# Kernel optimization log

Measured on AMD Instinct MI355X. Metric: run time of the kernel, lower is better.

Reference implementation:

```python
import jax, jax.numpy as jnp
import numpy as np

B_, N, C = 1024, 64, 512
H = 16          # num_heads
NW = 64         # number of windows (B_ % NW == 0)


def setup_inputs() -> dict:
    key = jax.random.key(0)
    ks = jax.random.split(key, 7)
    return {
        "x": jax.random.normal(ks[0], (B_, N, C), jnp.float32),
        "mask": jax.random.normal(ks[1], (NW, N, N), jnp.float32),
        "qkv_w": jax.random.normal(ks[2], (C, 3 * C), jnp.float32) * 0.02,
        "qkv_b": jax.random.normal(ks[3], (3 * C,), jnp.float32) * 0.02,
        "proj_w": jax.random.normal(ks[4], (C, C), jnp.float32) * 0.02,
        "proj_b": jax.random.normal(ks[5], (C,), jnp.float32) * 0.02,
        "bias_table": jax.random.normal(ks[6], (2 * N - 1, H), jnp.float32) * 0.02,
    }


def reference(x, mask, qkv_w, qkv_b, proj_w, proj_b, bias_table):
    b_, n, c = x.shape
    h = bias_table.shape[1]
    ws = (bias_table.shape[0] + 1) // 2  # window_size, == n here
    d = c // h
    scale = d ** -0.5

    qkv = x @ qkv_w + qkv_b                                   # [B_, N, 3C]
    qkv = qkv.reshape(b_, n, 3, h, d).transpose(2, 0, 3, 1, 4)  # [3, B_, H, N, d]
    q, k, v = qkv[0] * scale, qkv[1], qkv[2]

    attn = jnp.einsum('bhnd,bhmd->bhnm', q, k)                # [B_, H, N, N]

    coords = jnp.arange(ws)
    rel_idx = coords[:, None] - coords[None, :] + ws - 1       # [ws, ws]
    bias = bias_table[rel_idx].transpose(2, 0, 1)              # [H, ws, ws]
    attn = attn + bias[None]

    nw = mask.shape[0]
    attn = attn.reshape(b_ // nw, nw, h, n, n) + mask[None, :, None]
    attn = attn.reshape(-1, h, n, n)
    attn = jax.nn.softmax(attn, axis=-1)

    out = jnp.einsum('bhnm,bhmd->bhnd', attn, v)               # [B_, H, N, d]
    # Faithful to the TF code: v keeps a leading singleton dim after tf.split,
    # so attn@v is [1, B_, H, N, d]; perm [0,2,1,3,4] swaps B_ and H before
    # the final reshape to (B_, N, C).
    out = out[None].transpose(0, 2, 1, 3, 4).reshape(b_, n, c)
    return out @ proj_w + proj_b
```

## Files before the change

kernel.cpp:

```cpp
#include <hip/hip_runtime.h>
#include <hip/hip_bf16.h>
#include <stdint.h>

typedef __attribute__((ext_vector_type(4))) float f32x4;
typedef __attribute__((ext_vector_type(8))) short s16x8;

__device__ __forceinline__ short f2bf(float f) {
  union { float f; uint32_t u; } v; v.f = f;
  uint32_t r = v.u + 0x7FFFu + ((v.u >> 16) & 1u);
  return (short)(r >> 16);
}

__device__ __forceinline__ void async16(const void* g, void* l) {
  __builtin_amdgcn_global_load_lds(
      (const __attribute__((address_space(1))) void*)g,
      (__attribute__((address_space(3))) void*)l, 16, 0, 0);
}

__global__ __launch_bounds__(256) void k_cast_bf16(const float* __restrict__ in,
                                                   short* __restrict__ out, int n8) {
  int i = blockIdx.x * 256 + threadIdx.x;
  if (i >= n8) return;
  const float4* p = (const float4*)in + (size_t)i * 2;
  float4 a = p[0], b = p[1];
  s16x8 o;
  o[0] = f2bf(a.x); o[1] = f2bf(a.y); o[2] = f2bf(a.z); o[3] = f2bf(a.w);
  o[4] = f2bf(b.x); o[5] = f2bf(b.y); o[6] = f2bf(b.z); o[7] = f2bf(b.w);
  ((s16x8*)out)[i] = o;
}

__global__ __launch_bounds__(256) void k_transpose_cast(const float* __restrict__ in,
                                                        short* __restrict__ out,
                                                        int K, int N) {
  __shared__ float tile[64][65];
  const int bx = blockIdx.x;
  const int by = blockIdx.y;
  const int tx = threadIdx.x & 63, ty = threadIdx.x >> 6;
#pragma unroll
  for (int r = ty; r < 64; r += 4)
    tile[r][tx] = in[(size_t)(by * 64 + r) * N + bx * 64 + tx];
  __syncthreads();
#pragma unroll
  for (int r = ty; r < 64; r += 4)
    out[(size_t)(bx * 64 + r) * K + by * 64 + tx] = f2bf(tile[tx][r]);
}

#define TILE_SH 16384

template <bool F32OUT, int NBN>
__global__ __launch_bounds__(512, 2) void k_gemm256p(const short* __restrict__ A,
                                                     const short* __restrict__ Bw,
                                                     const float* __restrict__ bias,
                                                     void* __restrict__ C,
                                                     int N, int K, int nrounds) {
  __shared__ short lds[2 * 2 * TILE_SH];
  const int t = threadIdx.x;
  const int w = t >> 6, l = t & 63;
  const int wm = w >> 2, wn = w & 3;
  const int swz = (((int)blockIdx.x & 7) << 5) + ((int)blockIdx.x >> 3);

  const int NT = 8;
  const int NS = nrounds * NT;

  auto stage = [&](const short* __restrict__ G, int row0, int kt, short* dst) {
#pragma unroll
    for (int L = 0; L < 2; ++L) {
      int cw = L * 512 + (t & ~63);
      int c = cw + l;
      int r = c >> 3, s = c & 7;
      async16(G + (size_t)(row0 + r) * K + kt + ((s ^ (r & 7)) << 3), dst + cw * 8);
    }
  };
  auto issueA = [&](int step, int bmv, int hf) {
    int kt = step & 7;
    stage(A, bmv * 256 + hf * 128, kt * 64, lds + (kt & 1) * 32768 + hf * 8192);
  };
  auto issueB = [&](int step, int bnv, int hf) {
    int kt = step & 7;
    stage(Bw, bnv * 256 + hf * 128, kt * 64, lds + (kt & 1) * 32768 + TILE_SH + hf * 8192);
  };

  const int g = l >> 4, v = l & 7;
  int ofsA[2], ofsB[2];
#pragma unroll
  for (int ks = 0; ks < 2; ++ks) {
    ofsA[ks] = (wm * 128 + (l & 15)) * 64 + (((ks * 4 + g) ^ v) << 3);
    ofsB[ks] = (wn * 64 + (l & 15)) * 64 + (((ks * 4 + g) ^ v) << 3);
  }

  f32x4 acc[8][4] = {};
  s16x8 bfr[4][2];

  {
    const int bm0 = swz / NBN, bn0 = swz % NBN;
    issueB(0, bn0, 0); issueB(0, bn0, 1);
    issueA(0, bm0, 0); issueA(0, bm0, 1);
    issueB(1, bn0, 0); issueB(1, bn0, 1);
  }
  asm volatile("s_waitcnt vmcnt(4)" ::: "memory");
  __builtin_amdgcn_s_barrier();

#define PHASE(AI0, STAGE_STMT, TAIL_STMT)                                                                      \
  {                                                                                                            \
    s16x8 a00 = *(const s16x8*)(Ab + ofsA[0] + (AI0) * 1024);                                                  \
    s16x8 a01 = *(const s16x8*)(Ab + ofsA[1] + (AI0) * 1024);                                                  \
    s16x8 a10 = *(const s16x8*)(Ab + ofsA[0] + ((AI0) + 1) * 1024);                                            \
    s16x8 a11 = *(const s16x8*)(Ab + ofsA[1] + ((AI0) + 1) * 1024);                                            \
    STAGE_STMT;                                                                                                \
    __builtin_amdgcn_s_barrier();                                                                              \
    asm volatile("s_waitcnt lgkmcnt(0)" ::: "memory");                                                         \
    __builtin_amdgcn_s_setprio(1);                                                                             \
    _Pragma("unroll")                                                                                          \
    for (int nj = 0; nj < 4; ++nj) {                                                                           \
      acc[(AI0)][nj] = __builtin_amdgcn_mfma_f32_16x16x32_bf16(a00, bfr[nj][0], acc[(AI0)][nj], 0, 0, 0);      \
      acc[(AI0)][nj] = __builtin_amdgcn_mfma_f32_16x16x32_bf16(a01, bfr[nj][1], acc[(AI0)][nj], 0, 0, 0);      \
      acc[(AI0) + 1][nj] = __builtin_amdgcn_mfma_f32_16x16x32_bf16(a10, bfr[nj][0], acc[(AI0) + 1][nj], 0, 0, 0); \
      acc[(AI0) + 1][nj] = __builtin_amdgcn_mfma_f32_16x16x32_bf16(a11, bfr[nj][1], acc[(AI0) + 1][nj], 0, 0, 0); \
    }                                                                                                          \
    __builtin_amdgcn_s_setprio(0);                                                                             \
    TAIL_STMT;                                                                                                 \
    __builtin_amdgcn_s_barrier();                                                                              \
  }

  for (int j = 0; j < nrounds; ++j) {
    const int tauc = swz + (j << 8);
    const int bmc = tauc / NBN, bnc = tauc % NBN;
    for (int T = 0; T < NT; ++T) {
      const int s = (j << 3) + T;
      const int s1 = s + 1, s2 = s + 2;
      const int tau1 = swz + (((s1) >> 3) << 8);
      const int tau2 = swz + (((s2) >> 3) << 8);
      const int bm1 = tau1 / NBN;
      const int bn2 = tau2 % NBN;
      const short* Ab = lds + (T & 1) * 32768;
      const short* Bb = Ab + TILE_SH;
#pragma unroll
      for (int nj = 0; nj < 4; ++nj)
#pragma unroll
        for (int ks = 0; ks < 2; ++ks)
          bfr[nj][ks] = *(const s16x8*)(Bb + ofsB[ks] + nj * 1024);

      PHASE(0, if (s1 < NS) issueA(s1, bm1, 0), );
      PHASE(2, if (s1 < NS) issueA(s1, bm1, 1), );
      PHASE(4, if (s2 < NS) issueB(s2, bn2, 0), );
      PHASE(6, if (s2 < NS) issueB(s2, bn2, 1),
            if (s2 < NS) { asm volatile("s_waitcnt vmcnt(4)" ::: "memory"); }
            else if (s1 < NS) { asm volatile("s_waitcnt vmcnt(0)" ::: "memory"); });
    }

#pragma unroll
    for (int ai = 0; ai < 8; ++ai)
#pragma unroll
      for (int nj = 0; nj < 4; ++nj) {
        int col = bnc * 256 + wn * 64 + nj * 16 + (l & 15);
        float bv = bias[col];
#pragma unroll
        for (int r = 0; r < 4; ++r) {
          int row = bmc * 256 + wm * 128 + ai * 16 + (l >> 4) * 4 + r;
          float vv = acc[ai][nj][r] + bv;
          if (F32OUT)
            ((float*)C)[(size_t)row * N + col] = vv;
          else
            ((short*)C)[(size_t)row * N + col] = f2bf(vv);
        }
      }
#pragma unroll
    for (int ai = 0; ai < 8; ++ai)
#pragma unroll
      for (int nj = 0; nj < 4; ++nj)
        acc[ai][nj] = (f32x4){0.f, 0.f, 0.f, 0.f};
  }
#undef PHASE
}

__global__ __launch_bounds__(256) void k_attn(const short* __restrict__ qkv,
                                              const float* __restrict__ mask,
                                              const float* __restrict__ bias_table,
                                              short* __restrict__ Y) {
  __shared__ float mask_lds[64 * 64];
  __shared__ float bias_lds[4][128];
  __shared__ short p_lds[4][64][72];

  const int t = threadIdx.x, wv = t >> 6, ln = t & 63;
  const int b = blockIdx.x;
  const int h = blockIdx.y * 4 + wv;

  const float4* mk = (const float4*)(mask + (size_t)(b & 63) * 4096);
#pragma unroll
  for (int u = 0; u < 4; ++u)
    ((float4*)mask_lds)[t + 256 * u] = mk[t + 256 * u];
  for (int u = ln; u < 127; u += 64) bias_lds[wv][u] = bias_table[u * 16 + h];
  __syncthreads();

  const short* qb = qkv + (size_t)b * 64 * 1536 + h * 32;

  s16x8 qf[4], kf[4];
#pragma unroll
  for (int i = 0; i < 4; ++i) {
    qf[i] = *(const s16x8*)(qb + (size_t)(16 * i + (ln & 15)) * 1536 + (ln >> 4) * 8);
    kf[i] = *(const s16x8*)(qb + (size_t)(16 * i + (ln & 15)) * 1536 + 512 + (ln >> 4) * 8);
  }
  f32x4 s[4][4] = {};
#pragma unroll
  for (int i = 0; i < 4; ++i)
#pragma unroll
    for (int j = 0; j < 4; ++j)
      s[i][j] = __builtin_amdgcn_mfma_f32_16x16x32_bf16(qf[i], kf[j], s[i][j], 0, 0, 0);

  const float scale = 0.17677669529663687f;
#pragma unroll
  for (int i = 0; i < 4; ++i)
#pragma unroll
    for (int r = 0; r < 4; ++r) {
      int nn = 16 * i + (ln >> 4) * 4 + r;
      float vals[4];
      float vmax = -1e30f;
#pragma unroll
      for (int j = 0; j < 4; ++j) {
        int mm = 16 * j + (ln & 15);
        float x = s[i][j][r] * scale + bias_lds[wv][nn - mm + 63] + mask_lds[nn * 64 + mm];
        vals[j] = x;
        vmax = fmaxf(vmax, x);
      }
#pragma unroll
      for (int d = 1; d < 16; d <<= 1) vmax = fmaxf(vmax, __shfl_xor(vmax, d, 64));
      float sum = 0.f;
#pragma unroll
      for (int j = 0; j < 4; ++j) {
        float p = __expf(vals[j] - vmax);
        vals[j] = p;
        sum += p;
      }
#pragma unroll
      for (int d = 1; d < 16; d <<= 1) sum += __shfl_xor(sum, d, 64);
      float rsv = 1.0f / sum;
#pragma unroll
      for (int j = 0; j < 4; ++j)
        p_lds[wv][nn][16 * j + (ln & 15)] = f2bf(vals[j] * rsv);
    }

  const short* vg = qb + 1024;
  f32x4 o[4][2] = {};
#pragma unroll
  for (int kk = 0; kk < 2; ++kk) {
    s16x8 pa[4];
#pragma unroll
    for (int i2 = 0; i2 < 4; ++i2)
      pa[i2] = *(const s16x8*)&p_lds[wv][16 * i2 + (ln & 15)][kk * 32 + (ln >> 4) * 8];
#pragma unroll
    for (int j2 = 0; j2 < 2; ++j2) {
      s16x8 vf;
#pragma unroll
      for (int jj = 0; jj < 8; ++jj)
        vf[jj] = vg[(size_t)(kk * 32 + (ln >> 4) * 8 + jj) * 1536 + 16 * j2 + (ln & 15)];
#pragma unroll
      for (int i2 = 0; i2 < 4; ++i2)
        o[i2][j2] = __builtin_amdgcn_mfma_f32_16x16x32_bf16(pa[i2], vf, o[i2][j2], 0, 0, 0);
    }
  }

#pragma unroll
  for (int i2 = 0; i2 < 4; ++i2)
#pragma unroll
    for (int j2 = 0; j2 < 2; ++j2)
#pragma unroll
      for (int r = 0; r < 4; ++r) {
        int n = 16 * i2 + (ln >> 4) * 4 + r;
        int d = 16 * j2 + (ln & 15);
        int rr = h * 64 + (b >> 4);
        int ss = (b & 15) * 4 + (n >> 4);
        int cc = (n & 15) * 32 + d;
        Y[((size_t)rr * 64 + ss) * 512 + cc] = f2bf(o[i2][j2][r]);
      }
}

extern "C" void kernel_launch(void* const* d_in, const int* in_sizes, int n_in,
                              void* d_out, int out_size, void* d_ws, size_t ws_size,
                              hipStream_t stream) {
  const float* x      = (const float*)d_in[0];
  const float* mask   = (const float*)d_in[1];
  const float* qkv_w  = (const float*)d_in[2];
  const float* qkv_b  = (const float*)d_in[3];
  const float* proj_w = (const float*)d_in[4];
  const float* proj_b = (const float*)d_in[5];
  const float* btab   = (const float*)d_in[6];
  float* out = (float*)d_out;

  char* w = (char*)d_ws;
  short* qkv_ws = (short*)w;
  short* xbf    = (short*)(w + (size_t)65536 * 1536 * 2);
  short* Y      = xbf;
  short* wT     = (short*)(w + (size_t)65536 * 1536 * 2 + (size_t)65536 * 512 * 2);
  short* projT  = wT + 1536 * 512;

  k_cast_bf16<<<16384, 256, 0, stream>>>(x, xbf, 33554432 / 8);
  k_transpose_cast<<<dim3(24, 8), 256, 0, stream>>>(qkv_w, wT, 512, 1536);
  k_transpose_cast<<<dim3(8, 8), 256, 0, stream>>>(proj_w, projT, 512, 512);
  k_gemm256p<false, 6><<<256, 512, 0, stream>>>(xbf, wT, qkv_b, qkv_ws, 1536, 512, 6);
  k_attn<<<dim3(1024, 4), 256, 0, stream>>>(qkv_ws, mask, btab, Y);
  k_gemm256p<true, 2><<<256, 512, 0, stream>>>(Y, projT, proj_b, out, 512, 512, 2);
}
```

Before: 306.7 us.

## Restructure GEMM main loop into K-split half-tile double-buffered register pipeline

```diff
diff --git a/kernel.cpp b/kernel.cpp
--- a/kernel.cpp
+++ b/kernel.cpp
@@ -45,107 +45,100 @@
     out[(size_t)(bx * 64 + r) * K + by * 64 + tx] = f2bf(tile[tx][r]);
 }
 
-#define TILE_SH 16384
+#define RGN 16384
 
 template <bool F32OUT, int NBN>
-__global__ __launch_bounds__(512, 2) void k_gemm256p(const short* __restrict__ A,
-                                                     const short* __restrict__ Bw,
-                                                     const float* __restrict__ bias,
-                                                     void* __restrict__ C,
-                                                     int N, int K, int nrounds) {
-  __shared__ short lds[2 * 2 * TILE_SH];
+__global__ __launch_bounds__(512, 1) void k_gemmks(const short* __restrict__ A,
+                                                   const short* __restrict__ Bw,
+                                                   const float* __restrict__ bias,
+                                                   void* __restrict__ C,
+                                                   int N, int K, int nrounds) {
+  __shared__ short lds[4 * RGN];
   const int t = threadIdx.x;
   const int w = t >> 6, l = t & 63;
   const int wm = w >> 2, wn = w & 3;
   const int swz = (((int)blockIdx.x & 7) << 5) + ((int)blockIdx.x >> 3);
 
-  const int NT = 8;
-  const int NS = nrounds * NT;
-
-  auto stage = [&](const short* __restrict__ G, int row0, int kt, short* dst) {
+  const int laneOff = (l & 15) * 32 + (((l >> 4) ^ ((l >> 1) & 3)) << 3);
+
+  auto stageR = [&](int bmv, int bnv, int kt, int ks) {
+    short* base = lds + (((kt & 1) << 1) + ks) * RGN;
 #pragma unroll
     for (int L = 0; L < 2; ++L) {
-      int cw = L * 512 + (t & ~63);
-      int c = cw + l;
-      int r = c >> 3, s = c & 7;
-      async16(G + (size_t)(row0 + r) * K + kt + ((s ^ (r & 7)) << 3), dst + cw * 8);
+      int pc = L * 512 + t;
+      int pr = pc >> 2;
+      int gg = (pc & 3) ^ ((pr >> 1) & 3);
+      async16(A + (size_t)(bmv * 256 + pr) * K + kt * 64 + ks * 32 + gg * 8,
+              base + (L * 512 + (t & ~63)) * 8);
+    }
+#pragma unroll
+    for (int L = 0; L < 2; ++L) {
+      int pc = L * 512 + t;
+      int pr = pc >> 2;
+      int gg = (pc & 3) ^ ((pr >> 1) & 3);
+      async16(Bw + (size_t)(bnv * 256 + pr) * K + kt * 64 + ks * 32 + gg * 8,
+              base + 8192 + (L * 512 + (t & ~63)) * 8);
     }
   };
-  auto issueA = [&](int step, int bmv, int hf) {
-    int kt = step & 7;
-    stage(A, bmv * 256 + hf * 128, kt * 64, lds + (kt & 1) * 32768 + hf * 8192);
-  };
-  auto issueB = [&](int step, int bnv, int hf) {
-    int kt = step & 7;
-    stage(Bw, bnv * 256 + hf * 128, kt * 64, lds + (kt & 1) * 32768 + TILE_SH + hf * 8192);
-  };
-
-  const int g = l >> 4, v = l & 7;
-  int ofsA[2], ofsB[2];
-#pragma unroll
-  for (int ks = 0; ks < 2; ++ks) {
-    ofsA[ks] = (wm * 128 + (l & 15)) * 64 + (((ks * 4 + g) ^ v) << 3);
-    ofsB[ks] = (wn * 64 + (l & 15)) * 64 + (((ks * 4 + g) ^ v) << 3);
-  }
+
+#define RD_FRAGS(NA, NB, RIDX)                                                        \
+  _Pragma("unroll") for (int ai = 0; ai < 8; ++ai)                                    \
+      NA[ai] = *(const s16x8*)(lds + (RIDX) * RGN + (wm * 128 + ai * 16) * 32 + laneOff); \
+  _Pragma("unroll") for (int nj = 0; nj < 4; ++nj)                                    \
+      NB[nj] = *(const s16x8*)(lds + (RIDX) * RGN + 8192 + (wn * 64 + nj * 16) * 32 + laneOff);
+
+#define MFMAS(CA, CB)                                                                 \
+  __builtin_amdgcn_s_setprio(1);                                                      \
+  _Pragma("unroll") for (int nj = 0; nj < 4; ++nj)                                    \
+      _Pragma("unroll") for (int ai = 0; ai < 8; ++ai)                                \
+          acc[ai][nj] = __builtin_amdgcn_mfma_f32_16x16x32_bf16(CA[ai], CB[nj], acc[ai][nj], 0, 0, 0); \
+  __builtin_amdgcn_s_setprio(0);
 
   f32x4 acc[8][4] = {};
-  s16x8 bfr[4][2];
+  s16x8 Xa[8], Xb[4], Ya[8], Yb[4];
 
   {
-    const int bm0 = swz / NBN, bn0 = swz % NBN;
-    issueB(0, bn0, 0); issueB(0, bn0, 1);
-    issueA(0, bm0, 0); issueA(0, bm0, 1);
-    issueB(1, bn0, 0); issueB(1, bn0, 1);
-  }
-  asm volatile("s_waitcnt vmcnt(4)" ::: "memory");
+    const int tau0 = swz;
+    const int bm0 = tau0 / NBN, bn0 = tau0 % NBN;
+    stageR(bm0, bn0, 0, 0);
+    stageR(bm0, bn0, 0, 1);
+    stageR(bm0, bn0, 1, 0);
+    stageR(bm0, bn0, 1, 1);
+  }
+  asm volatile("s_waitcnt vmcnt(8)" ::: "memory");
   __builtin_amdgcn_s_barrier();
-
-#define PHASE(AI0, STAGE_STMT, TAIL_STMT)                                                                      \
-  {                                                                                                            \
-    s16x8 a00 = *(const s16x8*)(Ab + ofsA[0] + (AI0) * 1024);                                                  \
-    s16x8 a01 = *(const s16x8*)(Ab + ofsA[1] + (AI0) * 1024);                                                  \
-    s16x8 a10 = *(const s16x8*)(Ab + ofsA[0] + ((AI0) + 1) * 1024);                                            \
-    s16x8 a11 = *(const s16x8*)(Ab + ofsA[1] + ((AI0) + 1) * 1024);                                            \
-    STAGE_STMT;                                                                                                \
-    __builtin_amdgcn_s_barrier();                                                                              \
-    asm volatile("s_waitcnt lgkmcnt(0)" ::: "memory");                                                         \
-    __builtin_amdgcn_s_setprio(1);                                                                             \
-    _Pragma("unroll")                                                                                          \
-    for (int nj = 0; nj < 4; ++nj) {                                                                           \
-      acc[(AI0)][nj] = __builtin_amdgcn_mfma_f32_16x16x32_bf16(a00, bfr[nj][0], acc[(AI0)][nj], 0, 0, 0);      \
-      acc[(AI0)][nj] = __builtin_amdgcn_mfma_f32_16x16x32_bf16(a01, bfr[nj][1], acc[(AI0)][nj], 0, 0, 0);      \
-      acc[(AI0) + 1][nj] = __builtin_amdgcn_mfma_f32_16x16x32_bf16(a10, bfr[nj][0], acc[(AI0) + 1][nj], 0, 0, 0); \
-      acc[(AI0) + 1][nj] = __builtin_amdgcn_mfma_f32_16x16x32_bf16(a11, bfr[nj][1], acc[(AI0) + 1][nj], 0, 0, 0); \
-    }                                                                                                          \
-    __builtin_amdgcn_s_setprio(0);                                                                             \
-    TAIL_STMT;                                                                                                 \
-    __builtin_amdgcn_s_barrier();                                                                              \
-  }
+  RD_FRAGS(Xa, Xb, 0);
+  asm volatile("s_waitcnt lgkmcnt(0)" ::: "memory");
 
   for (int j = 0; j < nrounds; ++j) {
-    const int tauc = swz + (j << 8);
-    const int bmc = tauc / NBN, bnc = tauc % NBN;
-    for (int T = 0; T < NT; ++T) {
-      const int s = (j << 3) + T;
-      const int s1 = s + 1, s2 = s + 2;
-      const int tau1 = swz + (((s1) >> 3) << 8);
-      const int tau2 = swz + (((s2) >> 3) << 8);
-      const int bm1 = tau1 / NBN;
-      const int bn2 = tau2 % NBN;
-      const short* Ab = lds + (T & 1) * 32768;
-      const short* Bb = Ab + TILE_SH;
-#pragma unroll
-      for (int nj = 0; nj < 4; ++nj)
-#pragma unroll
-        for (int ks = 0; ks < 2; ++ks)
-          bfr[nj][ks] = *(const s16x8*)(Bb + ofsB[ks] + nj * 1024);
-
-      PHASE(0, if (s1 < NS) issueA(s1, bm1, 0), );
-      PHASE(2, if (s1 < NS) issueA(s1, bm1, 1), );
-      PHASE(4, if (s2 < NS) issueB(s2, bn2, 0), );
-      PHASE(6, if (s2 < NS) issueB(s2, bn2, 1),
-            if (s2 < NS) { asm volatile("s_waitcnt vmcnt(4)" ::: "memory"); }
-            else if (s1 < NS) { asm volatile("s_waitcnt vmcnt(0)" ::: "memory"); });
+    const int tau = swz + (j << 8);
+    const int bmc = tau / NBN, bnc = tau % NBN;
+    const int tau1 = tau + 256;
+    const int bm1 = tau1 / NBN, bn1 = tau1 % NBN;
+    const bool more = (j + 1) < nrounds;
+
+#pragma unroll
+    for (int k = 0; k < 8; ++k) {
+      const int skt = (k + 2) & 7;
+      const int sbm = (k < 6) ? bmc : bm1;
+      const int sbn = (k < 6) ? bnc : bn1;
+      const bool sg = (k < 6) ? true : more;
+      asm volatile("s_waitcnt vmcnt(8)" ::: "memory");
+      __builtin_amdgcn_s_barrier();
+      RD_FRAGS(Ya, Yb, ((k & 1) << 1) + 1);
+      if (sg) stageR(sbm, sbn, skt, 0);
+      __builtin_amdgcn_sched_barrier(0);
+      MFMAS(Xa, Xb);
+      asm volatile("s_waitcnt lgkmcnt(0)" ::: "memory");
+      __builtin_amdgcn_sched_barrier(0);
+      asm volatile("s_waitcnt vmcnt(8)" ::: "memory");
+      __builtin_amdgcn_s_barrier();
+      if (k < 7 || more) { RD_FRAGS(Xa, Xb, (((k + 1) & 1) << 1)); }
+      if (sg) stageR(sbm, sbn, skt, 1);
+      __builtin_amdgcn_sched_barrier(0);
+      MFMAS(Ya, Yb);
+      asm volatile("s_waitcnt lgkmcnt(0)" ::: "memory");
+      __builtin_amdgcn_sched_barrier(0);
     }
 
 #pragma unroll
@@ -170,7 +163,8 @@
       for (int nj = 0; nj < 4; ++nj)
         acc[ai][nj] = (f32x4){0.f, 0.f, 0.f, 0.f};
   }
-#undef PHASE
+#undef RD_FRAGS
+#undef MFMAS
 }
 
 __global__ __launch_bounds__(256) void k_attn(const short* __restrict__ qkv,
@@ -296,7 +290,7 @@
   k_cast_bf16<<<16384, 256, 0, stream>>>(x, xbf, 33554432 / 8);
   k_transpose_cast<<<dim3(24, 8), 256, 0, stream>>>(qkv_w, wT, 512, 1536);
   k_transpose_cast<<<dim3(8, 8), 256, 0, stream>>>(proj_w, projT, 512, 512);
-  k_gemm256p<false, 6><<<256, 512, 0, stream>>>(xbf, wT, qkv_b, qkv_ws, 1536, 512, 6);
+  k_gemmks<false, 6><<<256, 512, 0, stream>>>(xbf, wT, qkv_b, qkv_ws, 1536, 512, 6);
   k_attn<<<dim3(1024, 4), 256, 0, stream>>>(qkv_ws, mask, btab, Y);
-  k_gemm256p<true, 2><<<256, 512, 0, stream>>>(Y, projT, proj_b, out, 512, 512, 2);
-}
+  k_gemmks<true, 2><<<256, 512, 0, stream>>>(Y, projT, proj_b, out, 512, 512, 2);
+}
```

Result: slower. 577.6 us (+88.3%).

## Transpose attention MFMA layout, stage V in LDS, vectorize stores

Applied to the files above, without the earlier changes.

```diff
diff --git a/kernel.cpp b/kernel.cpp
--- a/kernel.cpp
+++ b/kernel.cpp
@@ -9,6 +9,9 @@
   union { float f; uint32_t u; } v; v.f = f;
   uint32_t r = v.u + 0x7FFFu + ((v.u >> 16) & 1u);
   return (short)(r >> 16);
+}
+__device__ __forceinline__ uint32_t pack2bf(float a, float b) {
+  return (uint32_t)(uint16_t)f2bf(a) | ((uint32_t)(uint16_t)f2bf(b) << 16);
 }
 
 __device__ __forceinline__ void async16(const void* g, void* l) {
@@ -47,19 +50,19 @@
 
 #define TILE_SH 16384
 
-template <bool F32OUT, int NBN>
+template <bool F32OUT, int NBN, int KK>
 __global__ __launch_bounds__(512, 2) void k_gemm256p(const short* __restrict__ A,
                                                      const short* __restrict__ Bw,
                                                      const float* __restrict__ bias,
                                                      void* __restrict__ C,
-                                                     int N, int K, int nrounds) {
+                                                     int N, int nrounds) {
   __shared__ short lds[2 * 2 * TILE_SH];
   const int t = threadIdx.x;
   const int w = t >> 6, l = t & 63;
   const int wm = w >> 2, wn = w & 3;
   const int swz = (((int)blockIdx.x & 7) << 5) + ((int)blockIdx.x >> 3);
 
-  const int NT = 8;
+  const int NT = KK >> 6;
   const int NS = nrounds * NT;
 
   auto stage = [&](const short* __restrict__ G, int row0, int kt, short* dst) {
@@ -68,7 +71,7 @@
       int cw = L * 512 + (t & ~63);
       int c = cw + l;
       int r = c >> 3, s = c & 7;
-      async16(G + (size_t)(row0 + r) * K + kt + ((s ^ (r & 7)) << 3), dst + cw * 8);
+      async16(G + (size_t)(row0 + r) * KK + kt + ((s ^ (r & 7)) << 3), dst + cw * 8);
     }
   };
   auto issueA = [&](int step, int bmv, int hf) {
@@ -180,98 +183,112 @@
   __shared__ float mask_lds[64 * 64];
   __shared__ float bias_lds[4][128];
   __shared__ short p_lds[4][64][72];
+  __shared__ short v_lds[4][64][40];
 
   const int t = threadIdx.x, wv = t >> 6, ln = t & 63;
   const int b = blockIdx.x;
   const int h = blockIdx.y * 4 + wv;
+  const int hi = ln >> 4, lo = ln & 15;
 
   const float4* mk = (const float4*)(mask + (size_t)(b & 63) * 4096);
 #pragma unroll
-  for (int u = 0; u < 4; ++u)
-    ((float4*)mask_lds)[t + 256 * u] = mk[t + 256 * u];
+  for (int u = 0; u < 4; ++u) {
+    int idx = t + 256 * u;
+    int row = idx >> 4, c4 = (idx & 15) * 4;
+    *(float4*)&mask_lds[row * 64 + (c4 ^ ((row & 7) << 2))] = mk[idx];
+  }
   for (int u = ln; u < 127; u += 64) bias_lds[wv][u] = bias_table[u * 16 + h];
+
+  const short* qb = qkv + (size_t)b * 64 * 1536 + h * 32;
+  const short* vg = qb + 1024;
+#pragma unroll
+  for (int u = 0; u < 4; ++u) {
+    int row = u * 16 + (ln >> 2), c8 = (ln & 3) * 8;
+    *(s16x8*)&v_lds[wv][row][c8] = *(const s16x8*)(vg + (size_t)row * 1536 + c8);
+  }
   __syncthreads();
 
-  const short* qb = qkv + (size_t)b * 64 * 1536 + h * 32;
-
   s16x8 qf[4], kf[4];
 #pragma unroll
   for (int i = 0; i < 4; ++i) {
-    qf[i] = *(const s16x8*)(qb + (size_t)(16 * i + (ln & 15)) * 1536 + (ln >> 4) * 8);
-    kf[i] = *(const s16x8*)(qb + (size_t)(16 * i + (ln & 15)) * 1536 + 512 + (ln >> 4) * 8);
-  }
-  f32x4 s[4][4] = {};
-#pragma unroll
-  for (int i = 0; i < 4; ++i)
+    qf[i] = *(const s16x8*)(qb + (size_t)(16 * i + lo) * 1536 + hi * 8);
+    kf[i] = *(const s16x8*)(qb + (size_t)(16 * i + lo) * 1536 + 512 + hi * 8);
+  }
+  f32x4 s2[4][4] = {};
+#pragma unroll
+  for (int j = 0; j < 4; ++j)
+#pragma unroll
+    for (int i = 0; i < 4; ++i)
+      s2[j][i] = __builtin_amdgcn_mfma_f32_16x16x32_bf16(kf[j], qf[i], s2[j][i], 0, 0, 0);
+
+  const float scale = 0.17677669529663687f;
+#pragma unroll
+  for (int i = 0; i < 4; ++i) {
+    const int n = 16 * i + lo;
+    const int msw = (n & 7) << 2;
+    float x[16];
+    float vmax = -1e30f;
 #pragma unroll
     for (int j = 0; j < 4; ++j)
-      s[i][j] = __builtin_amdgcn_mfma_f32_16x16x32_bf16(qf[i], kf[j], s[i][j], 0, 0, 0);
-
-  const float scale = 0.17677669529663687f;
-#pragma unroll
-  for (int i = 0; i < 4; ++i)
-#pragma unroll
-    for (int r = 0; r < 4; ++r) {
-      int nn = 16 * i + (ln >> 4) * 4 + r;
-      float vals[4];
-      float vmax = -1e30f;
-#pragma unroll
-      for (int j = 0; j < 4; ++j) {
-        int mm = 16 * j + (ln & 15);
-        float x = s[i][j][r] * scale + bias_lds[wv][nn - mm + 63] + mask_lds[nn * 64 + mm];
-        vals[j] = x;
-        vmax = fmaxf(vmax, x);
+#pragma unroll
+      for (int r = 0; r < 4; ++r) {
+        int m = 16 * j + 4 * hi + r;
+        float xx = s2[j][i][r] * scale + bias_lds[wv][n - m + 63] +
+                   mask_lds[n * 64 + (m ^ msw)];
+        x[j * 4 + r] = xx;
+        vmax = fmaxf(vmax, xx);
       }
-#pragma unroll
-      for (int d = 1; d < 16; d <<= 1) vmax = fmaxf(vmax, __shfl_xor(vmax, d, 64));
-      float sum = 0.f;
-#pragma unroll
-      for (int j = 0; j < 4; ++j) {
-        float p = __expf(vals[j] - vmax);
-        vals[j] = p;
-        sum += p;
-      }
-#pragma unroll
-      for (int d = 1; d < 16; d <<= 1) sum += __shfl_xor(sum, d, 64);
-      float rsv = 1.0f / sum;
-#pragma unroll
-      for (int j = 0; j < 4; ++j)
-        p_lds[wv][nn][16 * j + (ln & 15)] = f2bf(vals[j] * rsv);
-    }
-
-  const short* vg = qb + 1024;
-  f32x4 o[4][2] = {};
+    vmax = fmaxf(vmax, __shfl_xor(vmax, 16, 64));
+    vmax = fmaxf(vmax, __shfl_xor(vmax, 32, 64));
+    float sum = 0.f;
+#pragma unroll
+    for (int u = 0; u < 16; ++u) {
+      x[u] = __expf(x[u] - vmax);
+      sum += x[u];
+    }
+    sum += __shfl_xor(sum, 16, 64);
+    sum += __shfl_xor(sum, 32, 64);
+    float rsv = 1.0f / sum;
+#pragma unroll
+    for (int j = 0; j < 4; ++j)
+#pragma unroll
+      for (int rp = 0; rp < 2; ++rp)
+        *(uint32_t*)&p_lds[wv][n][16 * j + 4 * hi + rp * 2] =
+            pack2bf(x[j * 4 + rp * 2] * rsv, x[j * 4 + rp * 2 + 1] * rsv);
+  }
+
+  f32x4 o2[2][4] = {};
 #pragma unroll
   for (int kk = 0; kk < 2; ++kk) {
     s16x8 pa[4];
 #pragma unroll
     for (int i2 = 0; i2 < 4; ++i2)
-      pa[i2] = *(const s16x8*)&p_lds[wv][16 * i2 + (ln & 15)][kk * 32 + (ln >> 4) * 8];
+      pa[i2] = *(const s16x8*)&p_lds[wv][16 * i2 + lo][kk * 32 + hi * 8];
 #pragma unroll
     for (int j2 = 0; j2 < 2; ++j2) {
       s16x8 vf;
 #pragma unroll
       for (int jj = 0; jj < 8; ++jj)
-        vf[jj] = vg[(size_t)(kk * 32 + (ln >> 4) * 8 + jj) * 1536 + 16 * j2 + (ln & 15)];
+        vf[jj] = v_lds[wv][kk * 32 + hi * 8 + jj][16 * j2 + lo];
 #pragma unroll
       for (int i2 = 0; i2 < 4; ++i2)
-        o[i2][j2] = __builtin_amdgcn_mfma_f32_16x16x32_bf16(pa[i2], vf, o[i2][j2], 0, 0, 0);
-    }
-  }
-
-#pragma unroll
-  for (int i2 = 0; i2 < 4; ++i2)
-#pragma unroll
-    for (int j2 = 0; j2 < 2; ++j2)
-#pragma unroll
-      for (int r = 0; r < 4; ++r) {
-        int n = 16 * i2 + (ln >> 4) * 4 + r;
-        int d = 16 * j2 + (ln & 15);
-        int rr = h * 64 + (b >> 4);
-        int ss = (b & 15) * 4 + (n >> 4);
-        int cc = (n & 15) * 32 + d;
-        Y[((size_t)rr * 64 + ss) * 512 + cc] = f2bf(o[i2][j2][r]);
-      }
+        o2[j2][i2] = __builtin_amdgcn_mfma_f32_16x16x32_bf16(vf, pa[i2], o2[j2][i2], 0, 0, 0);
+    }
+  }
+
+  const int rr = h * 64 + (b >> 4);
+#pragma unroll
+  for (int i2 = 0; i2 < 4; ++i2) {
+    int ss = (b & 15) * 4 + i2;
+    short* yr = Y + ((size_t)rr * 64 + ss) * 512 + lo * 32 + 4 * hi;
+#pragma unroll
+    for (int j2 = 0; j2 < 2; ++j2) {
+      uint2 pk;
+      pk.x = pack2bf(o2[j2][i2][0], o2[j2][i2][1]);
+      pk.y = pack2bf(o2[j2][i2][2], o2[j2][i2][3]);
+      *(uint2*)(yr + 16 * j2) = pk;
+    }
+  }
 }
 
 extern "C" void kernel_launch(void* const* d_in, const int* in_sizes, int n_in,
@@ -296,7 +313,7 @@
   k_cast_bf16<<<16384, 256, 0, stream>>>(x, xbf, 33554432 / 8);
   k_transpose_cast<<<dim3(24, 8), 256, 0, stream>>>(qkv_w, wT, 512, 1536);
   k_transpose_cast<<<dim3(8, 8), 256, 0, stream>>>(proj_w, projT, 512, 512);
-  k_gemm256p<false, 6><<<256, 512, 0, stream>>>(xbf, wT, qkv_b, qkv_ws, 1536, 512, 6);
+  k_gemm256p<false, 6, 512><<<256, 512, 0, stream>>>(xbf, wT, qkv_b, qkv_ws, 1536, 6);
   k_attn<<<dim3(1024, 4), 256, 0, stream>>>(qkv_ws, mask, btab, Y);
-  k_gemm256p<true, 2><<<256, 512, 0, stream>>>(Y, projT, proj_b, out, 512, 512, 2);
-}
+  k_gemm256p<true, 2, 512><<<256, 512, 0, stream>>>(Y, projT, proj_b, out, 512, 2);
+}
```

After: 290.5 us. -5.3%, faster.
